# Optimization experiments

Measured on AMD Instinct MI355X. Metric: run time of the kernel, lower is better.

The kernel has to match this reference:

```python
import jax, jax.numpy as jnp
import numpy as np

B, S, D = 16, 4096, 1024
DIM_K, DIM_V, NUM_HEAD = 1024, 1024, 16


def setup_inputs() -> dict:
    key = jax.random.key(0)
    ks = jax.random.split(key, 7)
    s_in = 1.0 / np.sqrt(D)
    return {
        "x": jax.random.normal(ks[0], (B, S, D), dtype=jnp.float32),
        "Wq": jax.random.normal(ks[1], (D, DIM_K), dtype=jnp.float32) * s_in,
        "bq": jnp.zeros((DIM_K,), dtype=jnp.float32),
        "Wk": jax.random.normal(ks[2], (D, DIM_K), dtype=jnp.float32) * s_in,
        "bk": jnp.zeros((DIM_K,), dtype=jnp.float32),
        "Wv": jax.random.normal(ks[3], (D, DIM_V), dtype=jnp.float32) * s_in,
        "bv": jnp.zeros((DIM_V,), dtype=jnp.float32),
    }


def reference(x, Wq, bq, Wk, bk, Wv, bv):
    H = NUM_HEAD
    b, s, _ = x.shape
    Q = x @ Wq + bq                      # (B,S,dim_k)
    K = x @ Wk + bk                      # (B,S,dim_k)
    V = x @ Wv + bv                      # (B,S,dim_v)
    Q_ = Q.reshape(b, s, H, DIM_K // H)  # (B,S,H,dk)
    K_ = K.reshape(b, s, H, DIM_K // H)
    V_ = V.reshape(b, s, H, DIM_V // H)
    # NOTE: faithful to the source quirk — scores are across HEADS (H x H)
    # at each (batch, seq) position; no 1/sqrt(dim_k) scaling (unused in source).
    scores = jnp.einsum("bshd,bsgd->bshg", Q_, K_)   # (B,S,H,H)
    atten = jax.nn.softmax(scores, axis=-1)
    out = jnp.einsum("bshg,bsgd->bshd", atten, V_)    # (B,S,H,dv_head)
    return out.reshape(b, s, -1)                      # (B,S,dim_v)
```

## Files before the change

### kernel.cpp

```cpp
#include <hip/hip_runtime.h>
#include <stdint.h>

#define M_TOTAL 65536
#define DIM     1024
#define NQKV    3072
#define NHEAD   16
#define HDIM    64

typedef __attribute__((ext_vector_type(8))) _Float16 f16x8;
typedef __attribute__((ext_vector_type(4))) _Float16 f16x4;
typedef __attribute__((ext_vector_type(4))) float    f32x4;

__global__ __launch_bounds__(256) void cvt_x_kernel(const float* __restrict__ x,
                                                    _Float16* __restrict__ xh,
                                                    int n4) {
    int i = blockIdx.x * blockDim.x + threadIdx.x;
    int stride = gridDim.x * blockDim.x;
    const float4* x4 = (const float4*)x;
    f16x4* o4 = (f16x4*)xh;
    for (; i < n4; i += stride) {
        float4 v = x4[i];
        f16x4 o;
        o[0] = (_Float16)v.x; o[1] = (_Float16)v.y;
        o[2] = (_Float16)v.z; o[3] = (_Float16)v.w;
        o4[i] = o;
    }
}

__global__ void cvt_w_kernel(const float* __restrict__ Wq,
                             const float* __restrict__ Wk,
                             const float* __restrict__ Wv,
                             _Float16* __restrict__ Wt) {
    __shared__ float tile[32][33];
    int which = blockIdx.z;
    const float* W = (which == 0) ? Wq : (which == 1) ? Wk : Wv;
    int d0 = blockIdx.y * 32, n0 = blockIdx.x * 32;
    int tx = threadIdx.x, ty = threadIdx.y;
    tile[ty][tx] = W[(size_t)(d0 + ty) * DIM + n0 + tx];
    __syncthreads();
    Wt[(size_t)(which * DIM + n0 + ty) * DIM + d0 + tx] = (_Float16)tile[tx][ty];
}

__global__ __launch_bounds__(256) void bias_kernel(const float* __restrict__ bq,
                                                   const float* __restrict__ bk,
                                                   const float* __restrict__ bv,
                                                   float* __restrict__ bias) {
    int i = blockIdx.x * 256 + threadIdx.x;
    if (i < NQKV)
        bias[i] = (i < 1024) ? bq[i] : (i < 2048) ? bk[i - 1024] : bv[i - 2048];
}

#define BM 128
#define BN 128
#define BK 32

__global__ __launch_bounds__(256) void qkv_gemm_kernel(const _Float16* __restrict__ Xh,
                                                       const _Float16* __restrict__ Wth,
                                                       const float* __restrict__ bias,
                                                       _Float16* __restrict__ Ch) {
    __shared__ _Float16 As[BM * BK];
    __shared__ _Float16 Bs[BN * BK];

    const int bid  = blockIdx.x;
    const int tn   = bid % (NQKV / BN);
    const int tm   = bid / (NQKV / BN);
    const int brow = tm * BM;
    const int bcol = tn * BN;

    const int tid = threadIdx.x;
    const int w   = tid >> 6;
    const int l   = tid & 63;
    const int wr  = w >> 1, wc = w & 1;

    const int lrow = l >> 2;
    const int lcg  = l & 3;

    f32x4 acc[4][4] = {};

    for (int k0 = 0; k0 < DIM; k0 += BK) {
#pragma unroll
        for (int is = 0; is < 2; ++is) {
            const int r = is * 64 + w * 16 + lrow;
            const _Float16* srcA = Xh  + (size_t)(brow + r) * DIM + k0 + lcg * 8;
            const _Float16* srcB = Wth + (size_t)(bcol + r) * DIM + k0 + lcg * 8;
            _Float16* dstA = As + (is * 64 + w * 16) * BK;
            _Float16* dstB = Bs + (is * 64 + w * 16) * BK;
            __builtin_amdgcn_global_load_lds((const __attribute__((address_space(1))) void*)srcA,
                                             (__attribute__((address_space(3))) void*)dstA, 16, 0, 0);
            __builtin_amdgcn_global_load_lds((const __attribute__((address_space(1))) void*)srcB,
                                             (__attribute__((address_space(3))) void*)dstB, 16, 0, 0);
        }
        __syncthreads();

        f16x8 af[4], bfr[4];
#pragma unroll
        for (int mi = 0; mi < 4; ++mi)
            af[mi] = *(const f16x8*)(As + (wr * 64 + mi * 16 + (l & 15)) * BK + (l >> 4) * 8);
#pragma unroll
        for (int ni = 0; ni < 4; ++ni)
            bfr[ni] = *(const f16x8*)(Bs + (wc * 64 + ni * 16 + (l & 15)) * BK + (l >> 4) * 8);
#pragma unroll
        for (int mi = 0; mi < 4; ++mi)
#pragma unroll
            for (int ni = 0; ni < 4; ++ni)
                acc[mi][ni] = __builtin_amdgcn_mfma_f32_16x16x32_f16(af[mi], bfr[ni], acc[mi][ni], 0, 0, 0);
        __syncthreads();
    }

#pragma unroll
    for (int ni = 0; ni < 4; ++ni) {
        const int col = bcol + wc * 64 + ni * 16 + (l & 15);
        const float bv = bias[col];
#pragma unroll
        for (int mi = 0; mi < 4; ++mi) {
#pragma unroll
            for (int j = 0; j < 4; ++j) {
                const int row = brow + wr * 64 + mi * 16 + (l >> 4) * 4 + j;
                Ch[(size_t)row * NQKV + col] = (_Float16)(acc[mi][ni][j] + bv);
            }
        }
    }
}

__global__ __launch_bounds__(256) void attn_kernel(const _Float16* __restrict__ QKVh,
                                                   float* __restrict__ out) {
    __shared__ _Float16 vlds[4][1024];
    __shared__ float attlds[4][16][16];

    const int w = threadIdx.x >> 6, l = threadIdx.x & 63;
    const size_t p = (size_t)blockIdx.x * 4 + w;
    const _Float16* base = QKVh + p * NQKV;
    const _Float16* qrow = base;
    const _Float16* krow = base + 1024;
    const _Float16* vrow = base + 2048;
    const int h = l & 15;
    const int g4 = (l >> 4) * 4;

    *(uint4*)&vlds[w][l * 16]     = *(const uint4*)&vrow[l * 16];
    *(uint4*)&vlds[w][l * 16 + 8] = *(const uint4*)&vrow[l * 16 + 8];

    const int fo = (l & 15) * HDIM + (l >> 4) * 8;
    f16x8 aK0 = *(const f16x8*)&krow[fo];
    f16x8 aK1 = *(const f16x8*)&krow[fo + 32];
    f16x8 bQ0 = *(const f16x8*)&qrow[fo];
    f16x8 bQ1 = *(const f16x8*)&qrow[fo + 32];

    f32x4 sT = {0.f, 0.f, 0.f, 0.f};
    sT = __builtin_amdgcn_mfma_f32_16x16x32_f16(aK0, bQ0, sT, 0, 0, 0);
    sT = __builtin_amdgcn_mfma_f32_16x16x32_f16(aK1, bQ1, sT, 0, 0, 0);

    float m = fmaxf(fmaxf(sT[0], sT[1]), fmaxf(sT[2], sT[3]));
    m = fmaxf(m, __shfl_xor(m, 16));
    m = fmaxf(m, __shfl_xor(m, 32));
    float e0 = __expf(sT[0] - m), e1 = __expf(sT[1] - m);
    float e2 = __expf(sT[2] - m), e3 = __expf(sT[3] - m);
    float s = e0 + e1 + e2 + e3;
    s += __shfl_xor(s, 16);
    s += __shfl_xor(s, 32);
    const float inv = 1.0f / s;

    float4 att = make_float4(e0 * inv, e1 * inv, e2 * inv, e3 * inv);
    *(float4*)&attlds[w][h][g4] = att;
    __syncthreads();

    const int dbase = (l >> 4) * 16;
    float acc[16];
#pragma unroll
    for (int c = 0; c < 16; ++c) acc[c] = 0.f;

#pragma unroll
    for (int g = 0; g < 16; ++g) {
        const float a = attlds[w][h][g];
        f16x8 v0 = *(const f16x8*)&vlds[w][g * HDIM + dbase];
        f16x8 v1 = *(const f16x8*)&vlds[w][g * HDIM + dbase + 8];
#pragma unroll
        for (int c = 0; c < 8; ++c) {
            acc[c]     += a * (float)v0[c];
            acc[c + 8] += a * (float)v1[c];
        }
    }

    float* op = out + p * DIM + h * HDIM + dbase;
#pragma unroll
    for (int c = 0; c < 16; c += 4)
        *(float4*)(op + c) = make_float4(acc[c], acc[c + 1], acc[c + 2], acc[c + 3]);
}

extern "C" void kernel_launch(void* const* d_in, const int* in_sizes, int n_in,
                              void* d_out, int out_size, void* d_ws, size_t ws_size,
                              hipStream_t stream) {
    const float* x  = (const float*)d_in[0];
    const float* Wq = (const float*)d_in[1];
    const float* bq = (const float*)d_in[2];
    const float* Wk = (const float*)d_in[3];
    const float* bk = (const float*)d_in[4];
    const float* Wv = (const float*)d_in[5];
    const float* bv = (const float*)d_in[6];
    float* out = (float*)d_out;

    char* ws = (char*)d_ws;
    _Float16* Xh  = (_Float16*)ws;
    _Float16* Wth = (_Float16*)(ws + 134217728);
    float*    bias = (float*)(ws + 134217728 + 6291456);
    _Float16* Ch  = (_Float16*)(ws + 134217728 + 6291456 + 12288);

    hipLaunchKernelGGL(cvt_x_kernel, dim3(2048), dim3(256), 0, stream,
                       x, Xh, (M_TOTAL * DIM) / 4);
    hipLaunchKernelGGL(cvt_w_kernel, dim3(32, 32, 3), dim3(32, 32), 0, stream,
                       Wq, Wk, Wv, Wth);
    hipLaunchKernelGGL(bias_kernel, dim3(12), dim3(256), 0, stream,
                       bq, bk, bv, bias);
    hipLaunchKernelGGL(qkv_gemm_kernel, dim3((M_TOTAL / BM) * (NQKV / BN)), dim3(256), 0, stream,
                       Xh, Wth, bias, Ch);
    hipLaunchKernelGGL(attn_kernel, dim3(M_TOTAL / 4), dim3(256), 0, stream,
                       Ch, out);
}
```

Baseline: 759.0 us.

## Rewrite QKV GEMM as 256x256 double-buffered, swizzled-LDS pipelined kernel

Replaces the 128x128 single-buffered QKV GEMM with a 256x256 tile and 512 threads. It double-buffers LDS (128 KB dynamic) with BK=64, XOR-swizzles the LDS layout, and interleaves global->LDS loads with MFMA quarters using explicit barriers, waitcnt and setprio. It also remaps block IDs for L2 locality. The aim is to hide load latency and raise MFMA utilization in the dominant GEMM. The cost is fragile hand scheduling, heavy LDS use that allows only a couple of blocks per CU, and many barriers.

```diff
diff --git a/kernel.cpp b/kernel.cpp
--- a/kernel.cpp
+++ b/kernel.cpp
@@ -50,73 +50,193 @@
         bias[i] = (i < 1024) ? bq[i] : (i < 2048) ? bk[i - 1024] : bv[i - 2048];
 }
 
-#define BM 128
-#define BN 128
-#define BK 32
-
-__global__ __launch_bounds__(256) void qkv_gemm_kernel(const _Float16* __restrict__ Xh,
-                                                       const _Float16* __restrict__ Wth,
-                                                       const float* __restrict__ bias,
-                                                       _Float16* __restrict__ Ch) {
-    __shared__ _Float16 As[BM * BK];
-    __shared__ _Float16 Bs[BN * BK];
-
-    const int bid  = blockIdx.x;
-    const int tn   = bid % (NQKV / BN);
-    const int tm   = bid / (NQKV / BN);
-    const int brow = tm * BM;
-    const int bcol = tn * BN;
+
+#define LDSA(slot)  ((slot) << 15)
+#define LDSB(slot)  (65536 + ((slot) << 15))
+
+#define MFMA_Q(MIBASE, NIBASE)                                                  \
+    __builtin_amdgcn_s_setprio(1);                                              \
+    _Pragma("unroll") for (int mi = 0; mi < 4; ++mi)                            \
+    _Pragma("unroll") for (int ni = 0; ni < 2; ++ni)                            \
+    _Pragma("unroll") for (int ks = 0; ks < 2; ++ks)                            \
+        acc[(MIBASE) + mi][(NIBASE) + ni] = __builtin_amdgcn_mfma_f32_16x16x32_f16( \
+            a[mi][ks], b[(NIBASE) + ni][ks], acc[(MIBASE) + mi][(NIBASE) + ni], 0, 0, 0); \
+    __builtin_amdgcn_s_setprio(0);
+
+__global__ __launch_bounds__(512, 2) void qkv_gemm_kernel(const _Float16* __restrict__ Xh,
+                                                          const _Float16* __restrict__ Wth,
+                                                          const float* __restrict__ bias,
+                                                          _Float16* __restrict__ Ch) {
+    extern __shared__ char smem[];
+
+    const int bid = blockIdx.x;
+    const int swz = (bid & 7) * (3072 / 8) + (bid >> 3);
+    const int tm  = swz / (NQKV / 256);
+    const int tn  = swz % (NQKV / 256);
+    const int brow = tm * 256;
+    const int bcol = tn * 256;
 
     const int tid = threadIdx.x;
     const int w   = tid >> 6;
     const int l   = tid & 63;
-    const int wr  = w >> 1, wc = w & 1;
-
-    const int lrow = l >> 2;
-    const int lcg  = l & 3;
-
-    f32x4 acc[4][4] = {};
-
-    for (int k0 = 0; k0 < DIM; k0 += BK) {
-#pragma unroll
-        for (int is = 0; is < 2; ++is) {
-            const int r = is * 64 + w * 16 + lrow;
-            const _Float16* srcA = Xh  + (size_t)(brow + r) * DIM + k0 + lcg * 8;
-            const _Float16* srcB = Wth + (size_t)(bcol + r) * DIM + k0 + lcg * 8;
-            _Float16* dstA = As + (is * 64 + w * 16) * BK;
-            _Float16* dstB = Bs + (is * 64 + w * 16) * BK;
-            __builtin_amdgcn_global_load_lds((const __attribute__((address_space(1))) void*)srcA,
-                                             (__attribute__((address_space(3))) void*)dstA, 16, 0, 0);
-            __builtin_amdgcn_global_load_lds((const __attribute__((address_space(1))) void*)srcB,
-                                             (__attribute__((address_space(3))) void*)dstB, 16, 0, 0);
-        }
-        __syncthreads();
-
-        f16x8 af[4], bfr[4];
-#pragma unroll
-        for (int mi = 0; mi < 4; ++mi)
-            af[mi] = *(const f16x8*)(As + (wr * 64 + mi * 16 + (l & 15)) * BK + (l >> 4) * 8);
-#pragma unroll
-        for (int ni = 0; ni < 4; ++ni)
-            bfr[ni] = *(const f16x8*)(Bs + (wc * 64 + ni * 16 + (l & 15)) * BK + (l >> 4) * 8);
-#pragma unroll
-        for (int mi = 0; mi < 4; ++mi)
-#pragma unroll
-            for (int ni = 0; ni < 4; ++ni)
-                acc[mi][ni] = __builtin_amdgcn_mfma_f32_16x16x32_f16(af[mi], bfr[ni], acc[mi][ni], 0, 0, 0);
-        __syncthreads();
-    }
-
+    const int wm  = w >> 2;
+    const int wn  = w & 3;
+
+    const int lrow8 = l >> 3;
+    const int lcol8 = (l & 7) ^ lrow8;
+    const _Float16* pAsrc = Xh  + (size_t)(brow + w * 8 + lrow8) * DIM + lcol8 * 8;
+    const _Float16* pBsrc = Wth + (size_t)(bcol + w * 8 + lrow8) * DIM + lcol8 * 8;
+
+    auto stA = [&](int slot, int kt, int half) {
+        const _Float16* s = pAsrc + ((size_t)half << 17) + ((size_t)kt << 6);
+        char* d = smem + LDSA(slot) + (half << 14) + (w << 10);
+        __builtin_amdgcn_global_load_lds((const __attribute__((address_space(1))) void*)s,
+                                         (__attribute__((address_space(3))) void*)d, 16, 0, 0);
+        __builtin_amdgcn_global_load_lds((const __attribute__((address_space(1))) void*)(s + (1 << 16)),
+                                         (__attribute__((address_space(3))) void*)(d + 8192), 16, 0, 0);
+    };
+    auto stB = [&](int slot, int kt, int half) {
+        const _Float16* s = pBsrc + ((size_t)half << 17) + ((size_t)kt << 6);
+        char* d = smem + LDSB(slot) + (half << 14) + (w << 10);
+        __builtin_amdgcn_global_load_lds((const __attribute__((address_space(1))) void*)s,
+                                         (__attribute__((address_space(3))) void*)d, 16, 0, 0);
+        __builtin_amdgcn_global_load_lds((const __attribute__((address_space(1))) void*)(s + (1 << 16)),
+                                         (__attribute__((address_space(3))) void*)(d + 8192), 16, 0, 0);
+    };
+
+    const int aRowB = ((wm << 7) + (l & 15)) << 7;
+    const int bRowB = 65536 + (((wn << 6) + (l & 15)) << 7);
+    const int xk0 = (((l >> 4) ^ (l & 7)) << 4);
+    const int xk1 = ((((l >> 4) + 4) ^ (l & 7)) << 4);
+    auto LDA = [&](int slot, int mi, int ks) -> f16x8 {
+        return *(const f16x8*)(smem + (slot << 15) + aRowB + (mi << 11) + (ks ? xk1 : xk0));
+    };
+    auto LDB = [&](int slot, int ni, int ks) -> f16x8 {
+        return *(const f16x8*)(smem + (slot << 15) + bRowB + (ni << 11) + (ks ? xk1 : xk0));
+    };
+
+    f32x4 acc[8][4] = {};
+    f16x8 a[4][2], b[4][2];
+
+    stB(0, 0, 0); stB(0, 0, 1);
+    stA(0, 0, 0); stA(0, 0, 1);
+    stB(1, 1, 0); stB(1, 1, 1);
+    asm volatile("s_waitcnt vmcnt(4)" ::: "memory");
+    __builtin_amdgcn_s_barrier();
+    __builtin_amdgcn_sched_barrier(0);
+
+#pragma unroll 1
+    for (int i = 0; i < 7; ++i) {
+        const int u = 2 * i;
+#pragma unroll
+        for (int mi = 0; mi < 4; ++mi) { a[mi][0] = LDA(0, mi, 0); a[mi][1] = LDA(0, mi, 1); }
+#pragma unroll
+        for (int ni = 0; ni < 2; ++ni) { b[ni][0] = LDB(0, ni, 0); b[ni][1] = LDB(0, ni, 1); }
+        stA(1, u + 1, 0);
+        __builtin_amdgcn_s_barrier();
+        MFMA_Q(0, 0)
+        __builtin_amdgcn_s_barrier();
+        b[2][0] = LDB(0, 2, 0); b[2][1] = LDB(0, 2, 1);
+        b[3][0] = LDB(0, 3, 0); b[3][1] = LDB(0, 3, 1);
+        stA(1, u + 1, 1);
+        __builtin_amdgcn_s_barrier();
+        MFMA_Q(0, 2)
+        __builtin_amdgcn_s_barrier();
+#pragma unroll
+        for (int mi = 0; mi < 4; ++mi) { a[mi][0] = LDA(0, mi + 4, 0); a[mi][1] = LDA(0, mi + 4, 1); }
+        stB(0, u + 2, 0);
+        __builtin_amdgcn_s_barrier();
+        MFMA_Q(4, 0)
+        __builtin_amdgcn_s_barrier();
+        stB(0, u + 2, 1);
+        asm volatile("s_waitcnt vmcnt(4)" ::: "memory");
+        __builtin_amdgcn_s_barrier();
+        __builtin_amdgcn_sched_barrier(0);
+        MFMA_Q(4, 2)
+        __builtin_amdgcn_s_barrier();
+#pragma unroll
+        for (int mi = 0; mi < 4; ++mi) { a[mi][0] = LDA(1, mi, 0); a[mi][1] = LDA(1, mi, 1); }
+#pragma unroll
+        for (int ni = 0; ni < 2; ++ni) { b[ni][0] = LDB(1, ni, 0); b[ni][1] = LDB(1, ni, 1); }
+        stA(0, u + 2, 0);
+        __builtin_amdgcn_s_barrier();
+        MFMA_Q(0, 0)
+        __builtin_amdgcn_s_barrier();
+        b[2][0] = LDB(1, 2, 0); b[2][1] = LDB(1, 2, 1);
+        b[3][0] = LDB(1, 3, 0); b[3][1] = LDB(1, 3, 1);
+        stA(0, u + 2, 1);
+        __builtin_amdgcn_s_barrier();
+        MFMA_Q(0, 2)
+        __builtin_amdgcn_s_barrier();
+#pragma unroll
+        for (int mi = 0; mi < 4; ++mi) { a[mi][0] = LDA(1, mi + 4, 0); a[mi][1] = LDA(1, mi + 4, 1); }
+        stB(1, u + 3, 0);
+        __builtin_amdgcn_s_barrier();
+        MFMA_Q(4, 0)
+        __builtin_amdgcn_s_barrier();
+        stB(1, u + 3, 1);
+        asm volatile("s_waitcnt vmcnt(4)" ::: "memory");
+        __builtin_amdgcn_s_barrier();
+        __builtin_amdgcn_sched_barrier(0);
+        MFMA_Q(4, 2)
+        __builtin_amdgcn_s_barrier();
+    }
+
+    {
+#pragma unroll
+        for (int mi = 0; mi < 4; ++mi) { a[mi][0] = LDA(0, mi, 0); a[mi][1] = LDA(0, mi, 1); }
+#pragma unroll
+        for (int ni = 0; ni < 2; ++ni) { b[ni][0] = LDB(0, ni, 0); b[ni][1] = LDB(0, ni, 1); }
+        stA(1, 15, 0);
+        __builtin_amdgcn_s_barrier();
+        MFMA_Q(0, 0)
+        __builtin_amdgcn_s_barrier();
+        b[2][0] = LDB(0, 2, 0); b[2][1] = LDB(0, 2, 1);
+        b[3][0] = LDB(0, 3, 0); b[3][1] = LDB(0, 3, 1);
+        stA(1, 15, 1);
+        __builtin_amdgcn_s_barrier();
+        MFMA_Q(0, 2)
+        __builtin_amdgcn_s_barrier();
+#pragma unroll
+        for (int mi = 0; mi < 4; ++mi) { a[mi][0] = LDA(0, mi + 4, 0); a[mi][1] = LDA(0, mi + 4, 1); }
+        __builtin_amdgcn_s_barrier();
+        MFMA_Q(4, 0)
+        __builtin_amdgcn_s_barrier();
+        asm volatile("s_waitcnt vmcnt(0)" ::: "memory");
+        __builtin_amdgcn_s_barrier();
+        __builtin_amdgcn_sched_barrier(0);
+        MFMA_Q(4, 2)
+        __builtin_amdgcn_s_barrier();
+#pragma unroll
+        for (int mi = 0; mi < 4; ++mi) { a[mi][0] = LDA(1, mi, 0); a[mi][1] = LDA(1, mi, 1); }
+#pragma unroll
+        for (int ni = 0; ni < 2; ++ni) { b[ni][0] = LDB(1, ni, 0); b[ni][1] = LDB(1, ni, 1); }
+        __builtin_amdgcn_s_barrier();
+        MFMA_Q(0, 0)
+        __builtin_amdgcn_s_barrier();
+        b[2][0] = LDB(1, 2, 0); b[2][1] = LDB(1, 2, 1);
+        b[3][0] = LDB(1, 3, 0); b[3][1] = LDB(1, 3, 1);
+        __builtin_amdgcn_s_barrier();
+        MFMA_Q(0, 2)
+        __builtin_amdgcn_s_barrier();
+#pragma unroll
+        for (int mi = 0; mi < 4; ++mi) { a[mi][0] = LDA(1, mi + 4, 0); a[mi][1] = LDA(1, mi + 4, 1); }
+        __builtin_amdgcn_s_barrier();
+        MFMA_Q(4, 0)
+        MFMA_Q(4, 2)
+    }
+
+    const int r4 = (l >> 4) << 2;
 #pragma unroll
     for (int ni = 0; ni < 4; ++ni) {
-        const int col = bcol + wc * 64 + ni * 16 + (l & 15);
+        const int col = bcol + (wn << 6) + (ni << 4) + (l & 15);
         const float bv = bias[col];
 #pragma unroll
-        for (int mi = 0; mi < 4; ++mi) {
-#pragma unroll
-            for (int j = 0; j < 4; ++j) {
-                const int row = brow + wr * 64 + mi * 16 + (l >> 4) * 4 + j;
-                Ch[(size_t)row * NQKV + col] = (_Float16)(acc[mi][ni][j] + bv);
+        for (int mi = 0; mi < 8; ++mi) {
+#pragma unroll
+            for (int jj = 0; jj < 4; ++jj) {
+                const int row = brow + (wm << 7) + (mi << 4) + r4 + jj;
+                Ch[(size_t)row * NQKV + col] = (_Float16)(acc[mi][ni][jj] + bv);
             }
         }
     }
@@ -170,13 +290,13 @@
 
 #pragma unroll
     for (int g = 0; g < 16; ++g) {
-        const float a = attlds[w][h][g];
+        const float av = attlds[w][h][g];
         f16x8 v0 = *(const f16x8*)&vlds[w][g * HDIM + dbase];
         f16x8 v1 = *(const f16x8*)&vlds[w][g * HDIM + dbase + 8];
 #pragma unroll
         for (int c = 0; c < 8; ++c) {
-            acc[c]     += a * (float)v0[c];
-            acc[c + 8] += a * (float)v1[c];
+            acc[c]     += av * (float)v0[c];
+            acc[c + 8] += av * (float)v1[c];
         }
     }
 
@@ -204,13 +324,17 @@
     float*    bias = (float*)(ws + 134217728 + 6291456);
     _Float16* Ch  = (_Float16*)(ws + 134217728 + 6291456 + 12288);
 
+    static int lds_attr_set = 0;
+    (void)hipFuncSetAttribute((const void*)qkv_gemm_kernel,
+                              hipFuncAttributeMaxDynamicSharedMemorySize, 131072);
+
     hipLaunchKernelGGL(cvt_x_kernel, dim3(2048), dim3(256), 0, stream,
                        x, Xh, (M_TOTAL * DIM) / 4);
     hipLaunchKernelGGL(cvt_w_kernel, dim3(32, 32, 3), dim3(32, 32), 0, stream,
                        Wq, Wk, Wv, Wth);
     hipLaunchKernelGGL(bias_kernel, dim3(12), dim3(256), 0, stream,
                        bq, bk, bv, bias);
-    hipLaunchKernelGGL(qkv_gemm_kernel, dim3((M_TOTAL / BM) * (NQKV / BN)), dim3(256), 0, stream,
+    hipLaunchKernelGGL(qkv_gemm_kernel, dim3((M_TOTAL / 256) * (NQKV / 256)), dim3(512), 131072, stream,
                        Xh, Wth, bias, Ch);
     hipLaunchKernelGGL(attn_kernel, dim3(M_TOTAL / 4), dim3(256), 0, stream,
                        Ch, out);
```

After: 638.5 us. -15.9%, faster.
